# Kernel tuning notes

Measured on AMD Instinct MI355X. Metric: run time of the kernel, lower is better.

Reference implementation:

```python
import jax, jax.numpy as jnp
import numpy as np

B, D, C = 4096, 128, 256


def setup_inputs() -> dict:
    key = jax.random.key(0)
    kx, km, kc = jax.random.split(key, 3)
    X = jax.random.normal(kx, (B, D), dtype=jnp.float32)
    means = jax.random.normal(km, (D, C), dtype=jnp.float32)
    # Build an SPD covariance and invert it (as the torch module does in __init__)
    A = jax.random.normal(kc, (D, D), dtype=jnp.float32)
    covar = A @ A.T / D + jnp.eye(D, dtype=jnp.float32)
    alpha = jnp.linalg.inv(covar)  # [D, D]
    return {"X": X, "means": means, "alpha": alpha}


def reference(X, means, alpha):
    # X: [B, D], means: [D, C], alpha: [D, D]
    d2 = X[:, :, None] - means[None, :, :]          # [B, D, C]
    # Quadratic form diagonal only: q[b,c] = d2[b,:,c]^T alpha d2[b,:,c]
    ad2 = jnp.einsum('de,bec->bdc', alpha, d2)       # [B, D, C]
    q = jnp.einsum('bdc,bdc->bc', d2, ad2)           # [B, C]
    return jnp.min(q, axis=1)                        # [B]
```

## Files before the change

kernel.cpp:

```cpp
#include <hip/hip_runtime.h>
#include <hip/hip_bf16.h>

constexpr int Bn = 4096;
constexpr int Dn = 128;
constexpr int Cn = 256;

typedef __attribute__((ext_vector_type(8))) short bf16x8;
typedef __attribute__((ext_vector_type(4))) float f32x4;

static __device__ inline unsigned short f2bfu(float f) {
    __hip_bfloat16 h = __float2bfloat16(f);
    return *reinterpret_cast<unsigned short*>(&h);
}
static __device__ inline float bfu2f(unsigned short u) {
    __hip_bfloat16 h = *reinterpret_cast<__hip_bfloat16*>(&u);
    return __bfloat162float(h);
}
static __device__ inline unsigned pk2(float x, float y) {
    return (unsigned)f2bfu(x) | ((unsigned)f2bfu(y) << 16);
}

#define SWZ_OFF(row, e) ((row) * 256 + ((((e) * 2)) ^ (((row) & 7) << 4)))
#define MD_OFF(c, q) ((c) * 256 + ((((q) ^ ((c) & 15))) << 3))

static __device__ inline bf16x8 md_row8(const unsigned char* base, int c, int q0) {
    uint2 lo = *(const uint2*)(base + MD_OFF(c, q0));
    uint2 hi = *(const uint2*)(base + MD_OFF(c, q0 + 1));
    uint4 u;
    u.x = lo.x; u.y = lo.y; u.z = hi.x; u.w = hi.y;
    return *(bf16x8*)&u;
}

__global__ __launch_bounds__(512) void fused_kernel(
    const float* __restrict__ X, const float* __restrict__ means,
    const float* __restrict__ alpha, float* __restrict__ out) {
    __shared__ __align__(16) unsigned char AL[Dn * 256];
    __shared__ __align__(16) unsigned char MD[Cn * 256];
    __shared__ __align__(16) unsigned char XL[16 * 256];
    __shared__ float TP[2][Cn];
    __shared__ float SMIN[8][16];
    __shared__ float SXAX[8][16];

    const int tid = threadIdx.x;
    const int w = tid >> 6;
    const int lane = tid & 63;
    const int l15 = lane & 15;
    const int lh = lane >> 4;
    const int b0 = blockIdx.x * 16;
    const int cg = w & 3;
    const int rg = w >> 2;

    {
        {
            float4 v = ((const float4*)(X + b0 * Dn))[tid];
            const int b = tid >> 5;
            const int e0 = (tid & 31) << 2;
            uint2 pk;
            pk.x = pk2(v.x, v.y); pk.y = pk2(v.z, v.w);
            *(uint2*)(XL + SWZ_OFF(b, e0)) = pk;
        }
        const float4* a4 = (const float4*)alpha;
        #pragma unroll
        for (int i = 0; i < 8; ++i) {
            int idx4 = tid + i * 512;
            int d = idx4 >> 5, e0 = (idx4 & 31) << 2;
            float4 v = a4[idx4];
            unsigned char* p = AL + SWZ_OFF(d, e0);
            *(unsigned*)p = pk2(v.x, v.y);
            *(unsigned*)(p + 4) = pk2(v.z, v.w);
        }
        const int cb = 8 * w + (lane & 7);
        const int db0 = lane >> 3;
        #pragma unroll
        for (int i = 0; i < 4; ++i) {
            const int db = db0 + 8 * i;
            float4 v0 = *(const float4*)&means[(4 * db + 0) * Cn + 4 * cb];
            float4 v1 = *(const float4*)&means[(4 * db + 1) * Cn + 4 * cb];
            float4 v2 = *(const float4*)&means[(4 * db + 2) * Cn + 4 * cb];
            float4 v3 = *(const float4*)&means[(4 * db + 3) * Cn + 4 * cb];
            uint2 pk;
            pk.x = pk2(v0.x, v1.x); pk.y = pk2(v2.x, v3.x);
            *(uint2*)(MD + MD_OFF(4 * cb + 0, db)) = pk;
            pk.x = pk2(v0.y, v1.y); pk.y = pk2(v2.y, v3.y);
            *(uint2*)(MD + MD_OFF(4 * cb + 1, db)) = pk;
            pk.x = pk2(v0.z, v1.z); pk.y = pk2(v2.z, v3.z);
            *(uint2*)(MD + MD_OFF(4 * cb + 2, db)) = pk;
            pk.x = pk2(v0.w, v1.w); pk.y = pk2(v2.w, v3.w);
            *(uint2*)(MD + MD_OFF(4 * cb + 3, db)) = pk;
        }
    }
    __syncthreads();

    f32x4 gacc[4][4];
    #pragma unroll
    for (int j = 0; j < 4; ++j)
        #pragma unroll
        for (int s = 0; s < 4; ++s) gacc[j][s] = (f32x4){0.f, 0.f, 0.f, 0.f};
    f32x4 xacc = (f32x4){0.f, 0.f, 0.f, 0.f};
    bf16x8 af[4];

    #pragma unroll
    for (int k0 = 0; k0 < 4; ++k0) {
        af[k0] = *(const bf16x8*)(XL + SWZ_OFF(l15, 32 * k0 + 8 * lh));
        bf16x8 bj[4];
        #pragma unroll
        for (int j = 0; j < 4; ++j) {
            const int c = 64 * cg + 16 * j + l15;
            bj[j] = md_row8(MD, c, 8 * k0 + 2 * lh);
        }
        #pragma unroll
        for (int s = 0; s < 4; ++s) {
            const int mt = 4 * rg + s;
            bf16x8 a = *(const bf16x8*)(AL + SWZ_OFF(16 * mt + l15, 32 * k0 + 8 * lh));
            #pragma unroll
            for (int j = 0; j < 4; ++j)
                gacc[j][s] = __builtin_amdgcn_mfma_f32_16x16x32_bf16(a, bj[j], gacc[j][s], 0, 0, 0);
        }
        {
            bf16x8 aH = *(const bf16x8*)(AL + SWZ_OFF(16 * w + l15, 32 * k0 + 8 * lh));
            xacc = __builtin_amdgcn_mfma_f32_16x16x32_bf16(aH, af[k0], xacc, 0, 0, 0);
        }
    }

    {
        uint2 pk = *(const uint2*)(XL + SWZ_OFF(l15, 16 * w + 4 * lh));
        float v = bfu2f((unsigned short)(pk.x & 0xffffu)) * xacc[0];
        v = fmaf(bfu2f((unsigned short)(pk.x >> 16)),     xacc[1], v);
        v = fmaf(bfu2f((unsigned short)(pk.y & 0xffffu)), xacc[2], v);
        v = fmaf(bfu2f((unsigned short)(pk.y >> 16)),     xacc[3], v);
        v += __shfl_xor(v, 16);
        v += __shfl_xor(v, 32);
        if (lane < 16) SXAX[w][lane] = v;
    }

    {
        float tpart[4];
        #pragma unroll
        for (int j = 0; j < 4; ++j) {
            const int c = 64 * cg + 16 * j + l15;
            float v = 0.f;
            #pragma unroll
            for (int s = 0; s < 4; ++s) {
                const int mt = 4 * rg + s;
                uint2 mm = *(const uint2*)(MD + MD_OFF(c, 4 * mt + lh));
                v = fmaf(bfu2f((unsigned short)(mm.x & 0xffffu)), gacc[j][s][0], v);
                v = fmaf(bfu2f((unsigned short)(mm.x >> 16)),     gacc[j][s][1], v);
                v = fmaf(bfu2f((unsigned short)(mm.y & 0xffffu)), gacc[j][s][2], v);
                v = fmaf(bfu2f((unsigned short)(mm.y >> 16)),     gacc[j][s][3], v);
            }
            v += __shfl_xor(v, 16);
            v += __shfl_xor(v, 32);
            tpart[j] = v;
        }
        if (lane < 16)
            #pragma unroll
            for (int j = 0; j < 4; ++j) TP[rg][64 * cg + 16 * j + lane] = tpart[j];
    }
    __syncthreads();

    #pragma unroll
    for (int j = 0; j < 4; ++j) {
        const int c = 64 * cg + 16 * j + l15;
        #pragma unroll
        for (int s = 0; s < 4; ++s) {
            const int mt = 4 * rg + s;
            uint2 pk;
            pk.x = pk2(gacc[j][s][0], gacc[j][s][1]);
            pk.y = pk2(gacc[j][s][2], gacc[j][s][3]);
            *(uint2*)(MD + MD_OFF(c, 4 * mt + lh)) = pk;
        }
    }
    __syncthreads();

    bf16x8 bf2[2][4];
    #pragma unroll
    for (int j2 = 0; j2 < 2; ++j2) {
        const int rowc = 16 * (2 * w + j2) + l15;
        #pragma unroll
        for (int k0 = 0; k0 < 4; ++k0)
            bf2[j2][k0] = md_row8(MD, rowc, 8 * k0 + 2 * lh);
    }
    f32x4 macc[2];
    #pragma unroll
    for (int j2 = 0; j2 < 2; ++j2) macc[j2] = (f32x4){0.f, 0.f, 0.f, 0.f};
    #pragma unroll
    for (int k0 = 0; k0 < 4; ++k0)
        #pragma unroll
        for (int j2 = 0; j2 < 2; ++j2)
            macc[j2] = __builtin_amdgcn_mfma_f32_16x16x32_bf16(af[k0], bf2[j2][k0], macc[j2], 0, 0, 0);

    {
        float mr[4];
        #pragma unroll
        for (int r = 0; r < 4; ++r) mr[r] = 1e30f;
        #pragma unroll
        for (int j2 = 0; j2 < 2; ++j2) {
            const int c = 16 * (2 * w + j2) + l15;
            const float tc = TP[0][c] + TP[1][c];
            #pragma unroll
            for (int r = 0; r < 4; ++r)
                mr[r] = fminf(mr[r], tc - 2.f * macc[j2][r]);
        }
        #pragma unroll
        for (int r = 0; r < 4; ++r) {
            #pragma unroll
            for (int m = 1; m < 16; m <<= 1)
                mr[r] = fminf(mr[r], __shfl_xor(mr[r], m));
        }
        if (l15 == 0)
            #pragma unroll
            for (int r = 0; r < 4; ++r) SMIN[w][4 * lh + r] = mr[r];
    }
    __syncthreads();

    if (tid < 16) {
        float mnv = 1e30f, xa = 0.f;
        #pragma unroll
        for (int w8 = 0; w8 < 8; ++w8) {
            mnv = fminf(mnv, SMIN[w8][tid]);
            xa += SXAX[w8][tid];
        }
        out[b0 + tid] = xa + mnv;
    }
}

extern "C" void kernel_launch(void* const* d_in, const int* in_sizes, int n_in,
                              void* d_out, int out_size, void* d_ws, size_t ws_size,
                              hipStream_t stream) {
    const float* X     = (const float*)d_in[0];
    const float* means = (const float*)d_in[1];
    const float* alpha = (const float*)d_in[2];
    float* out = (float*)d_out;
    fused_kernel<<<Bn / 16, 512, 0, stream>>>(X, means, alpha, out);
}
```

Before: 11.50 us.

## Pipeline alpha and means staging across K-chunks to overlap loads with MFMA

```diff
diff --git a/kernel.cpp b/kernel.cpp
--- a/kernel.cpp
+++ b/kernel.cpp
@@ -50,46 +50,44 @@
     const int cg = w & 3;
     const int rg = w >> 2;
 
-    {
-        {
-            float4 v = ((const float4*)(X + b0 * Dn))[tid];
-            const int b = tid >> 5;
-            const int e0 = (tid & 31) << 2;
-            uint2 pk;
-            pk.x = pk2(v.x, v.y); pk.y = pk2(v.z, v.w);
-            *(uint2*)(XL + SWZ_OFF(b, e0)) = pk;
-        }
-        const float4* a4 = (const float4*)alpha;
-        #pragma unroll
-        for (int i = 0; i < 8; ++i) {
-            int idx4 = tid + i * 512;
-            int d = idx4 >> 5, e0 = (idx4 & 31) << 2;
-            float4 v = a4[idx4];
-            unsigned char* p = AL + SWZ_OFF(d, e0);
-            *(unsigned*)p = pk2(v.x, v.y);
-            *(unsigned*)(p + 4) = pk2(v.z, v.w);
-        }
-        const int cb = 8 * w + (lane & 7);
-        const int db0 = lane >> 3;
-        #pragma unroll
-        for (int i = 0; i < 4; ++i) {
-            const int db = db0 + 8 * i;
-            float4 v0 = *(const float4*)&means[(4 * db + 0) * Cn + 4 * cb];
-            float4 v1 = *(const float4*)&means[(4 * db + 1) * Cn + 4 * cb];
-            float4 v2 = *(const float4*)&means[(4 * db + 2) * Cn + 4 * cb];
-            float4 v3 = *(const float4*)&means[(4 * db + 3) * Cn + 4 * cb];
-            uint2 pk;
-            pk.x = pk2(v0.x, v1.x); pk.y = pk2(v2.x, v3.x);
-            *(uint2*)(MD + MD_OFF(4 * cb + 0, db)) = pk;
-            pk.x = pk2(v0.y, v1.y); pk.y = pk2(v2.y, v3.y);
-            *(uint2*)(MD + MD_OFF(4 * cb + 1, db)) = pk;
-            pk.x = pk2(v0.z, v1.z); pk.y = pk2(v2.z, v3.z);
-            *(uint2*)(MD + MD_OFF(4 * cb + 2, db)) = pk;
-            pk.x = pk2(v0.w, v1.w); pk.y = pk2(v2.w, v3.w);
-            *(uint2*)(MD + MD_OFF(4 * cb + 3, db)) = pk;
-        }
-    }
-    __syncthreads();
+    const int ad0 = tid >> 3;
+    const int ae0 = (tid & 7) << 2;
+    const int ad1 = (tid + 512) >> 3;
+    const int ae1 = ((tid + 512) & 7) << 2;
+    const int cb = 8 * w + (lane >> 3);
+    const int ebl = lane & 7;
+
+    float4 xv = ((const float4*)(X + b0 * Dn))[tid];
+    float4 a0 = *(const float4*)&alpha[ad0 * Dn + ae0];
+    float4 a1 = *(const float4*)&alpha[ad1 * Dn + ae1];
+    float4 m0 = *(const float4*)&means[(4 * ebl + 0) * Cn + 4 * cb];
+    float4 m1 = *(const float4*)&means[(4 * ebl + 1) * Cn + 4 * cb];
+    float4 m2 = *(const float4*)&means[(4 * ebl + 2) * Cn + 4 * cb];
+    float4 m3 = *(const float4*)&means[(4 * ebl + 3) * Cn + 4 * cb];
+
+    {
+        const int bq = tid >> 5, e0 = (tid & 31) << 2;
+        uint2 pk;
+        pk.x = pk2(xv.x, xv.y); pk.y = pk2(xv.z, xv.w);
+        *(uint2*)(XL + SWZ_OFF(bq, e0)) = pk;
+    }
+    {
+        unsigned char* p = AL + SWZ_OFF(ad0, ae0);
+        *(unsigned*)p = pk2(a0.x, a0.y); *(unsigned*)(p + 4) = pk2(a0.z, a0.w);
+        p = AL + SWZ_OFF(ad1, ae1);
+        *(unsigned*)p = pk2(a1.x, a1.y); *(unsigned*)(p + 4) = pk2(a1.z, a1.w);
+    }
+    {
+        uint2 pk;
+        pk.x = pk2(m0.x, m1.x); pk.y = pk2(m2.x, m3.x);
+        *(uint2*)(MD + MD_OFF(4 * cb + 0, ebl)) = pk;
+        pk.x = pk2(m0.y, m1.y); pk.y = pk2(m2.y, m3.y);
+        *(uint2*)(MD + MD_OFF(4 * cb + 1, ebl)) = pk;
+        pk.x = pk2(m0.z, m1.z); pk.y = pk2(m2.z, m3.z);
+        *(uint2*)(MD + MD_OFF(4 * cb + 2, ebl)) = pk;
+        pk.x = pk2(m0.w, m1.w); pk.y = pk2(m2.w, m3.w);
+        *(uint2*)(MD + MD_OFF(4 * cb + 3, ebl)) = pk;
+    }
 
     f32x4 gacc[4][4];
     #pragma unroll
@@ -101,6 +99,20 @@
 
     #pragma unroll
     for (int k0 = 0; k0 < 4; ++k0) {
+        __syncthreads();
+
+        float4 na0, na1, nm0, nm1, nm2, nm3;
+        if (k0 < 3) {
+            const int ke = 32 * (k0 + 1);
+            na0 = *(const float4*)&alpha[ad0 * Dn + ke + ae0];
+            na1 = *(const float4*)&alpha[ad1 * Dn + ke + ae1];
+            const int eb = 8 * (k0 + 1) + ebl;
+            nm0 = *(const float4*)&means[(4 * eb + 0) * Cn + 4 * cb];
+            nm1 = *(const float4*)&means[(4 * eb + 1) * Cn + 4 * cb];
+            nm2 = *(const float4*)&means[(4 * eb + 2) * Cn + 4 * cb];
+            nm3 = *(const float4*)&means[(4 * eb + 3) * Cn + 4 * cb];
+        }
+
         af[k0] = *(const bf16x8*)(XL + SWZ_OFF(l15, 32 * k0 + 8 * lh));
         bf16x8 bj[4];
         #pragma unroll
@@ -119,6 +131,24 @@
         {
             bf16x8 aH = *(const bf16x8*)(AL + SWZ_OFF(16 * w + l15, 32 * k0 + 8 * lh));
             xacc = __builtin_amdgcn_mfma_f32_16x16x32_bf16(aH, af[k0], xacc, 0, 0, 0);
+        }
+
+        if (k0 < 3) {
+            const int ke = 32 * (k0 + 1);
+            unsigned char* p = AL + SWZ_OFF(ad0, ke + ae0);
+            *(unsigned*)p = pk2(na0.x, na0.y); *(unsigned*)(p + 4) = pk2(na0.z, na0.w);
+            p = AL + SWZ_OFF(ad1, ke + ae1);
+            *(unsigned*)p = pk2(na1.x, na1.y); *(unsigned*)(p + 4) = pk2(na1.z, na1.w);
+            const int eb = 8 * (k0 + 1) + ebl;
+            uint2 pk;
+            pk.x = pk2(nm0.x, nm1.x); pk.y = pk2(nm2.x, nm3.x);
+            *(uint2*)(MD + MD_OFF(4 * cb + 0, eb)) = pk;
+            pk.x = pk2(nm0.y, nm1.y); pk.y = pk2(nm2.y, nm3.y);
+            *(uint2*)(MD + MD_OFF(4 * cb + 1, eb)) = pk;
+            pk.x = pk2(nm0.z, nm1.z); pk.y = pk2(nm2.z, nm3.z);
+            *(uint2*)(MD + MD_OFF(4 * cb + 2, eb)) = pk;
+            pk.x = pk2(nm0.w, nm1.w); pk.y = pk2(nm2.w, nm3.w);
+            *(uint2*)(MD + MD_OFF(4 * cb + 3, eb)) = pk;
         }
     }
 
```

Result: slower. 14.34 us (+24.8%).
